# Performance work log

Measured on AMD Instinct MI355X. Metric: run time of the kernel, lower is better.

## Reference

```python
import jax, jax.numpy as jnp
import numpy as np

D_MODEL = 1024
D_K = 64  # d_model // heads


def setup_inputs() -> dict:
    key = jax.random.key(0)
    ks = jax.random.split(key, 9)
    B, S = 8, 2048
    q = jax.random.normal(ks[0], (B, S, D_MODEL), dtype=jnp.float32)
    k = jax.random.normal(ks[1], (B, S, D_MODEL), dtype=jnp.float32)
    v = jax.random.normal(ks[2], (B, S, D_MODEL), dtype=jnp.float32)
    # Causal mask: True = blocked (masked_fill with -inf)
    mask = ~jnp.tril(jnp.ones((S, S), dtype=bool))
    # Linear params (stored as [in, out]); torch Linear init ~ U(-1/sqrt(in), 1/sqrt(in))
    lim = 1.0 / np.sqrt(D_MODEL)
    Wq = jax.random.uniform(ks[3], (D_MODEL, D_K), jnp.float32, -lim, lim)
    Wk = jax.random.uniform(ks[4], (D_MODEL, D_K), jnp.float32, -lim, lim)
    Wv = jax.random.uniform(ks[5], (D_MODEL, D_K), jnp.float32, -lim, lim)
    bq = jax.random.uniform(ks[6], (D_K,), jnp.float32, -lim, lim)
    bk = jax.random.uniform(ks[7], (D_K,), jnp.float32, -lim, lim)
    bv = jax.random.uniform(ks[8], (D_K,), jnp.float32, -lim, lim)
    return {"q": q, "k": k, "v": v, "mask": mask,
            "Wq": Wq, "bq": bq, "Wk": Wk, "bk": bk, "Wv": Wv, "bv": bv}


def reference(q, k, v, mask, Wq, bq, Wk, bk, Wv, bv):
    qp = q @ Wq + bq              # [B, S, d_k]
    kp = k @ Wk + bk              # [B, S, d_k]
    vp = v @ Wv + bv              # [B, S, d_k]
    scale = 1.0 / jnp.sqrt(jnp.float32(D_K))
    scores = jnp.einsum("bqd,bkd->bqk", qp, kp) * scale  # [B, S, S]
    scores = jnp.where(mask, -jnp.inf, scores)
    attn = jax.nn.softmax(scores, axis=-1)
    return jnp.einsum("bqk,bkd->bqd", attn, vp)  # [B, S, d_k]
```

## Files before the change

kernel.cpp:

```cpp
#include <hip/hip_runtime.h>
#include <hip/hip_bf16.h>

typedef short s4 __attribute__((ext_vector_type(4)));
typedef short s8 __attribute__((ext_vector_type(8)));
typedef float f4 __attribute__((ext_vector_type(4)));

#define MFMA16(a, b, c) __builtin_amdgcn_mfma_f32_16x16x16bf16_1k(a, b, c, 0, 0, 0)

__device__ __forceinline__ short f2bf(float f) {
    union { float f; unsigned u; } v; v.f = f;
    unsigned r = v.u + 0x7fffu + ((v.u >> 16) & 1u);
    return (short)(r >> 16);
}

struct ProjArgs {
    const float* X[3];
    const float* W[3];
    const float* b[3];
    unsigned short* O[3];
};

__global__ __launch_bounds__(256) void proj_kernel(ProjArgs args) {
    __shared__ short lA[64][68];
    __shared__ short lW[64][68];

    const int t  = threadIdx.x;
    const int wv = t >> 6, ln = t & 63, lg = ln >> 4, lr = ln & 15;
    const int which = blockIdx.y;

    const float* X = args.X[which] + (size_t)blockIdx.x * 64 * 1024;
    const float* W = args.W[which];

    f4 acc[4] = {f4{0,0,0,0}, f4{0,0,0,0}, f4{0,0,0,0}, f4{0,0,0,0}};

    for (int kk = 0; kk < 1024; kk += 64) {
        #pragma unroll
        for (int i = 0; i < 4; ++i) {
            int f  = t + i * 256;
            int r  = f >> 4;
            int c4 = f & 15;
            f4 a = *(const f4*)(X + (size_t)r * 1024 + kk + c4 * 4);
            f4 w = *(const f4*)(W + (size_t)(kk + r) * 64 + c4 * 4);
            s4 ab; ab[0]=f2bf(a[0]); ab[1]=f2bf(a[1]); ab[2]=f2bf(a[2]); ab[3]=f2bf(a[3]);
            s4 wb; wb[0]=f2bf(w[0]); wb[1]=f2bf(w[1]); wb[2]=f2bf(w[2]); wb[3]=f2bf(w[3]);
            *(s4*)&lA[r][c4 * 4] = ab;
            *(s4*)&lW[r][c4 * 4] = wb;
        }
        __syncthreads();

        #pragma unroll
        for (int ks = 0; ks < 4; ++ks) {
            s4 af = *(const s4*)&lA[wv * 16 + lr][ks * 16 + 4 * lg];
            #pragma unroll
            for (int nf = 0; nf < 4; ++nf) {
                s4 bf;
                #pragma unroll
                for (int e = 0; e < 4; ++e)
                    bf[e] = lW[ks * 16 + 4 * lg + e][nf * 16 + lr];
                acc[nf] = MFMA16(af, bf, acc[nf]);
            }
        }
        __syncthreads();
    }

    const float* bias = args.b[which];
    unsigned short* O = args.O[which];
    if (which == 2) {
        #pragma unroll
        for (int nf = 0; nf < 4; ++nf) {
            float bs = bias[nf * 16 + lr];
            int d = nf * 16 + lr;
            #pragma unroll
            for (int e = 0; e < 4; ++e) {
                int key = wv * 16 + 4 * lg + e;
                lA[d][key] = (short)f2bf(acc[nf][e] + bs);
            }
        }
        __syncthreads();
        const int grow0 = blockIdx.x * 64;
        unsigned short* tb = O + (size_t)(grow0 >> 11) * 131072
                               + (size_t)((grow0 & 2047) >> 6) * 4096;
        #pragma unroll
        for (int i = 0; i < 2; ++i) {
            int s = t * 2 + i;
            int d = s >> 3, k8 = s & 7;
            s8 v = *(const s8*)&lA[d][k8 * 8];
            *(s8*)(tb + (size_t)d * 64 + k8 * 8) = v;
        }
    } else {
        #pragma unroll
        for (int nf = 0; nf < 4; ++nf) {
            float bs = bias[nf * 16 + lr];
            int col = nf * 16 + lr;
            #pragma unroll
            for (int e = 0; e < 4; ++e) {
                int r = wv * 16 + 4 * lg + e;
                int grow = blockIdx.x * 64 + r;
                O[(size_t)grow * 64 + col] = (unsigned short)f2bf(acc[nf][e] + bs);
            }
        }
    }
}

__global__ __launch_bounds__(512) void attn_kernel(const unsigned short* __restrict__ qp,
                                                   const unsigned short* __restrict__ kp,
                                                   const unsigned short* __restrict__ vpT,
                                                   float* __restrict__ out) {
    __shared__ short lK[2][2][64][72];
    __shared__ short lV[2][2][64][72];

    const int t    = threadIdx.x;
    const int wave = t >> 6, ln = t & 63, lg = ln >> 4, lr = ln & 15;
    const int half = wave >> 2, hw = wave & 3;
    const int b = blockIdx.y, qt = blockIdx.x;
    const int qrow = qt * 64 + hw * 16 + lr;
    const int h = (qt + 2) >> 1;

    const int g = t >> 7, gi = t & 127, ghalf = g >> 1;
    const bool isV = (g & 1) != 0;
    const unsigned short* tb = (isV ? vpT : kp) + (size_t)b * 131072;

    const unsigned short* qpb = qp + (size_t)b * 131072;
    s4 qf[4];
    #pragma unroll
    for (int ks = 0; ks < 4; ++ks)
        qf[ks] = *(const s4*)(qpb + (size_t)qrow * 64 + ks * 16 + 4 * lg);

    f4 accO[4] = {f4{0,0,0,0}, f4{0,0,0,0}, f4{0,0,0,0}, f4{0,0,0,0}};
    float m = -3e38f, lsum = 0.f;

    s8 stg[4];
    {
        const unsigned short* p = tb + (size_t)(ghalf ? h : 0) * 4096;
        #pragma unroll
        for (int i = 0; i < 4; ++i)
            stg[i] = *(const s8*)(p + (gi + 128 * i) * 8);
    }

    int buf = 0;
    for (int j = 0; j < h; ++j) {
        {
            short (*dst)[72] = isV ? lV[ghalf][buf] : lK[ghalf][buf];
            #pragma unroll
            for (int i = 0; i < 4; ++i) {
                int s = gi + 128 * i;
                *(s8*)&dst[s >> 3][(s & 7) * 8] = stg[i];
            }
        }
        __syncthreads();

        if (j + 1 < h) {
            const unsigned short* p = tb + (size_t)((ghalf ? h : 0) + j + 1) * 4096;
            #pragma unroll
            for (int i = 0; i < 4; ++i)
                stg[i] = *(const s8*)(p + (gi + 128 * i) * 8);
        }

        const int kt = (half ? h : 0) + j;
        if (kt <= qt) {
            f4 st[4];
            #pragma unroll
            for (int kf = 0; kf < 4; ++kf) {
                f4 a = f4{0,0,0,0};
                #pragma unroll
                for (int ks = 0; ks < 4; ++ks) {
                    s4 kfr = *(const s4*)&lK[half][buf][kf * 16 + lr][ks * 16 + 4 * lg];
                    a = MFMA16(kfr, qf[ks], a);
                }
                st[kf] = a;
            }

            const bool diag = (kt == qt);
            const int kbase = kt * 64;
            float smax = -3e38f;
            #pragma unroll
            for (int kf = 0; kf < 4; ++kf) {
                #pragma unroll
                for (int e = 0; e < 4; ++e) {
                    float s = st[kf][e] * 0.125f;
                    if (diag && (kbase + kf * 16 + 4 * lg + e > qrow)) s = -3e38f;
                    st[kf][e] = s;
                    smax = fmaxf(smax, s);
                }
            }
            smax = fmaxf(smax, __shfl_xor(smax, 16));
            smax = fmaxf(smax, __shfl_xor(smax, 32));

            float mnew  = fmaxf(m, smax);
            float scale = __expf(m - mnew);
            float psum  = 0.f;
            s4 pf[4];
            #pragma unroll
            for (int kf = 0; kf < 4; ++kf) {
                f4 p;
                #pragma unroll
                for (int e = 0; e < 4; ++e) { p[e] = __expf(st[kf][e] - mnew); psum += p[e]; }
                s4 pb; pb[0]=f2bf(p[0]); pb[1]=f2bf(p[1]); pb[2]=f2bf(p[2]); pb[3]=f2bf(p[3]);
                pf[kf] = pb;
            }
            psum += __shfl_xor(psum, 16);
            psum += __shfl_xor(psum, 32);
            lsum = lsum * scale + psum;
            m = mnew;
            #pragma unroll
            for (int df = 0; df < 4; ++df) accO[df] *= scale;

            #pragma unroll
            for (int df = 0; df < 4; ++df) {
                #pragma unroll
                for (int kf = 0; kf < 4; ++kf) {
                    s4 vf = *(const s4*)&lV[half][buf][df * 16 + lr][kf * 16 + 4 * lg];
                    accO[df] = MFMA16(vf, pf[kf], accO[df]);
                }
            }
        }
        buf ^= 1;
    }

    __syncthreads();
    float* ex = (float*)&lK[0][0][0][0];
    const int idx = (hw * 64 + ln) * 19;
    if (half == 1) {
        ex[idx + 0] = m;
        ex[idx + 1] = lsum;
        #pragma unroll
        for (int df = 0; df < 4; ++df)
            #pragma unroll
            for (int e = 0; e < 4; ++e)
                ex[idx + 2 + df * 4 + e] = accO[df][e];
    }
    __syncthreads();
    if (half == 0) {
        float mB = ex[idx + 0], lB = ex[idx + 1];
        float mx = fmaxf(m, mB);
        float sA = __expf(m - mx), sB = __expf(mB - mx);
        float linv = 1.f / (lsum * sA + lB * sB);
        float* ob = out + ((size_t)b * 2048 + qrow) * 64;
        #pragma unroll
        for (int df = 0; df < 4; ++df) {
            f4 o;
            #pragma unroll
            for (int e = 0; e < 4; ++e)
                o[e] = (accO[df][e] * sA + ex[idx + 2 + df * 4 + e] * sB) * linv;
            *(f4*)(ob + df * 16 + 4 * lg) = o;
        }
    }
}

extern "C" void kernel_launch(void* const* d_in, const int* in_sizes, int n_in,
                              void* d_out, int out_size, void* d_ws, size_t ws_size,
                              hipStream_t stream) {
    const float* q  = (const float*)d_in[0];
    const float* k  = (const float*)d_in[1];
    const float* v  = (const float*)d_in[2];
    const float* Wq = (const float*)d_in[4];
    const float* bq = (const float*)d_in[5];
    const float* Wk = (const float*)d_in[6];
    const float* bk = (const float*)d_in[7];
    const float* Wv = (const float*)d_in[8];
    const float* bv = (const float*)d_in[9];

    unsigned short* qp  = (unsigned short*)d_ws;
    unsigned short* kp  = qp + (size_t)16384 * 64;
    unsigned short* vpT = kp + (size_t)16384 * 64;

    ProjArgs pa;
    pa.X[0] = q;  pa.X[1] = k;  pa.X[2] = v;
    pa.W[0] = Wq; pa.W[1] = Wk; pa.W[2] = Wv;
    pa.b[0] = bq; pa.b[1] = bk; pa.b[2] = bv;
    pa.O[0] = qp; pa.O[1] = kp; pa.O[2] = vpT;
    proj_kernel<<<dim3(256, 3), 256, 0, stream>>>(pa);

    attn_kernel<<<dim3(32, 8), 512, 0, stream>>>(qp, kp, vpT, (float*)d_out);
}
```

Baseline: 75.66 us.

## Double-buffer projection LDS tiles and prefetch next K-chunk into registers

The projection GEMM now stages the X and W tiles in two LDS buffers and issues the global loads for the next 64-wide K chunk into registers before running the MFMAs on the current chunk. This drops one barrier per iteration and overlaps global memory latency with compute. In exchange it doubles LDS use per block and holds extra prefetch registers, which may lower occupancy. The attention kernel is unchanged, so any effect is limited to the projection stage.

```diff
diff --git a/kernel.cpp b/kernel.cpp
--- a/kernel.cpp
+++ b/kernel.cpp
@@ -21,8 +21,8 @@
 };
 
 __global__ __launch_bounds__(256) void proj_kernel(ProjArgs args) {
-    __shared__ short lA[64][68];
-    __shared__ short lW[64][68];
+    __shared__ short lA[2][64][68];
+    __shared__ short lW[2][64][68];
 
     const int t  = threadIdx.x;
     const int wv = t >> 6, ln = t & 63, lg = ln >> 4, lr = ln & 15;
@@ -33,39 +33,59 @@
 
     f4 acc[4] = {f4{0,0,0,0}, f4{0,0,0,0}, f4{0,0,0,0}, f4{0,0,0,0}};
 
-    for (int kk = 0; kk < 1024; kk += 64) {
+    f4 xr[4], wr[4];
+#define PROJ_LOAD(kk)                                                         \
+    {                                                                         \
+        _Pragma("unroll")                                                     \
+        for (int i = 0; i < 4; ++i) {                                         \
+            int f  = t + i * 256;                                             \
+            int r  = f >> 4;                                                  \
+            int c4 = f & 15;                                                  \
+            xr[i] = *(const f4*)(X + (size_t)r * 1024 + (kk) + c4 * 4);       \
+            wr[i] = *(const f4*)(W + (size_t)((kk) + r) * 64 + c4 * 4);       \
+        }                                                                     \
+    }
+
+    PROJ_LOAD(0)
+
+    int buf = 0;
+    for (int j = 0; j < 16; ++j) {
         #pragma unroll
         for (int i = 0; i < 4; ++i) {
             int f  = t + i * 256;
             int r  = f >> 4;
             int c4 = f & 15;
-            f4 a = *(const f4*)(X + (size_t)r * 1024 + kk + c4 * 4);
-            f4 w = *(const f4*)(W + (size_t)(kk + r) * 64 + c4 * 4);
-            s4 ab; ab[0]=f2bf(a[0]); ab[1]=f2bf(a[1]); ab[2]=f2bf(a[2]); ab[3]=f2bf(a[3]);
-            s4 wb; wb[0]=f2bf(w[0]); wb[1]=f2bf(w[1]); wb[2]=f2bf(w[2]); wb[3]=f2bf(w[3]);
-            *(s4*)&lA[r][c4 * 4] = ab;
-            *(s4*)&lW[r][c4 * 4] = wb;
-        }
-        __syncthreads();
+            s4 ab; ab[0]=f2bf(xr[i][0]); ab[1]=f2bf(xr[i][1]);
+                   ab[2]=f2bf(xr[i][2]); ab[3]=f2bf(xr[i][3]);
+            s4 wb; wb[0]=f2bf(wr[i][0]); wb[1]=f2bf(wr[i][1]);
+                   wb[2]=f2bf(wr[i][2]); wb[3]=f2bf(wr[i][3]);
+            *(s4*)&lA[buf][r][c4 * 4] = ab;
+            *(s4*)&lW[buf][r][c4 * 4] = wb;
+        }
+        __syncthreads();
+
+        if (j < 15) PROJ_LOAD((j + 1) * 64)
 
         #pragma unroll
         for (int ks = 0; ks < 4; ++ks) {
-            s4 af = *(const s4*)&lA[wv * 16 + lr][ks * 16 + 4 * lg];
+            s4 af = *(const s4*)&lA[buf][wv * 16 + lr][ks * 16 + 4 * lg];
             #pragma unroll
             for (int nf = 0; nf < 4; ++nf) {
                 s4 bf;
                 #pragma unroll
                 for (int e = 0; e < 4; ++e)
-                    bf[e] = lW[ks * 16 + 4 * lg + e][nf * 16 + lr];
+                    bf[e] = lW[buf][ks * 16 + 4 * lg + e][nf * 16 + lr];
                 acc[nf] = MFMA16(af, bf, acc[nf]);
             }
         }
-        __syncthreads();
-    }
+        buf ^= 1;
+    }
+#undef PROJ_LOAD
 
     const float* bias = args.b[which];
     unsigned short* O = args.O[which];
     if (which == 2) {
+        __syncthreads();
         #pragma unroll
         for (int nf = 0; nf < 4; ++nf) {
             float bs = bias[nf * 16 + lr];
@@ -73,7 +93,7 @@
             #pragma unroll
             for (int e = 0; e < 4; ++e) {
                 int key = wv * 16 + 4 * lg + e;
-                lA[d][key] = (short)f2bf(acc[nf][e] + bs);
+                lA[0][d][key] = (short)f2bf(acc[nf][e] + bs);
             }
         }
         __syncthreads();
@@ -84,7 +104,7 @@
         for (int i = 0; i < 2; ++i) {
             int s = t * 2 + i;
             int d = s >> 3, k8 = s & 7;
-            s8 v = *(const s8*)&lA[d][k8 * 8];
+            s8 v = *(const s8*)&lA[0][d][k8 * 8];
             *(s8*)(tb + (size_t)d * 64 + k8 * 8) = v;
         }
     } else {
```

New measurement: 64.90 us. -14.2%, faster.
